# Performance work log

Measured on AMD Instinct MI355X. Metric: run time of the kernel, lower is better.

Reference implementation:

```python
import jax, jax.numpy as jnp
import numpy as np

SCALE = 20.0
EPS = 1e-8  # matches torch F.cosine_similarity eps


def _l2_normalize(x):
    # torch cosine_similarity clamps norms at eps
    norm = jnp.maximum(jnp.linalg.norm(x, axis=-1, keepdims=True), EPS)
    return x / norm


def setup_inputs() -> dict:
    key = jax.random.key(0)
    k1, k2 = jax.random.split(key)
    B, D = 4096, 1024
    anchor_emb = jax.random.normal(k1, (B, D), dtype=jnp.float32)
    pos_negs_emb = jax.random.normal(k2, (B, D), dtype=jnp.float32)
    return {"anchor_emb": anchor_emb, "pos_negs_emb": pos_negs_emb}


def reference(anchor_emb, pos_negs_emb):
    # cosine similarity as normalized GEMM (avoids (B,N,D) broadcast intermediate)
    a = _l2_normalize(anchor_emb)            # [B, D]
    p = _l2_normalize(pos_negs_emb)          # [N, D]
    scores = SCALE * jnp.einsum("bd,nd->bn", a, p)  # [B, N]
    B = scores.shape[0]
    # cross entropy with labels = arange(B): mean(logsumexp - diag)
    logZ = jax.scipy.special.logsumexp(scores, axis=1)  # [B]
    diag = scores[jnp.arange(B), jnp.arange(B)]          # [B]
    return jnp.mean(logZ - diag)
```

## Files before the change

### kernel.cpp

```cpp
#include <hip/hip_runtime.h>
#include <math.h>

#define NB 4096
#define ND 1024
#define SCALEF 20.0f
#define SQ 448.0f

typedef int intx4 __attribute__((ext_vector_type(4)));

__device__ __forceinline__ void load16_to_lds(const void* g, void* l) {
    __builtin_amdgcn_global_load_lds(
        (const __attribute__((address_space(1))) void*)g,
        (__attribute__((address_space(3))) void*)l, 16, 0, 0);
}

__device__ __forceinline__ int q8(float x) {
    float c = fminf(fmaxf(x, -127.0f), 127.0f);
    return (int)rintf(c);
}

__global__ __launch_bounds__(256) void mnrl_norm_cvt(
    const float* __restrict__ A, const float* __restrict__ P,
    signed char* __restrict__ Aq, signed char* __restrict__ Pq,
    float* __restrict__ rowsum, float* __restrict__ out) {
    if (blockIdx.x == 0 && threadIdx.x == 0) out[0] = 0.0f;
    int row = blockIdx.x * 4 + (threadIdx.x >> 6);
    int lane = threadIdx.x & 63;
    bool is_a = row < NB;
    const float* src = is_a ? (A + (size_t)row * ND)
                            : (P + (size_t)(row - NB) * ND);
    unsigned int* dst = (unsigned int*)(is_a ? (Aq + (size_t)row * ND)
                                             : (Pq + (size_t)(row - NB) * ND));

    float4 v[4];
    float ss = 0.0f;
#pragma unroll
    for (int i = 0; i < 4; ++i) {
        v[i] = ((const float4*)src)[i * 64 + lane];
        ss += v[i].x * v[i].x + v[i].y * v[i].y + v[i].z * v[i].z + v[i].w * v[i].w;
    }
#pragma unroll
    for (int off = 32; off > 0; off >>= 1) ss += __shfl_xor(ss, off, 64);
    float inv = SQ / fmaxf(sqrtf(ss), 1e-8f);
#pragma unroll
    for (int i = 0; i < 4; ++i) {
        int q0 = q8(v[i].x * inv), q1 = q8(v[i].y * inv);
        int q2 = q8(v[i].z * inv), q3 = q8(v[i].w * inv);
        dst[i * 64 + lane] = (unsigned int)((q0 & 255) | ((q1 & 255) << 8) |
                                            ((q2 & 255) << 16) | (q3 << 24));
    }
    if (is_a && lane == 0) rowsum[row] = 0.0f;
}

__global__ __launch_bounds__(512, 2) void mnrl_gemm_lse(
    const signed char* __restrict__ Aq, const signed char* __restrict__ Pq,
    float* __restrict__ rowsum, float* __restrict__ diag) {
    __shared__ __align__(16) unsigned char lds_a[2][256 * 128];
    __shared__ __align__(16) unsigned char lds_b[2][256 * 128];

    int bid = blockIdx.x;
    int swz = (bid & 7) * 32 + (bid >> 3);
    int tile_m = swz >> 4;
    int tile_n = swz & 15;

    int t = threadIdx.x;
    int lane = t & 63;
    int w = t >> 6;
    int wm = w >> 2;
    int wn = w & 3;
    int quad = lane >> 4;
    int l16 = lane & 15;

    const signed char* Abase = Aq + (size_t)tile_m * 256 * ND;
    const signed char* Pbase = Pq + (size_t)tile_n * 256 * ND;

    int srow = lane >> 3;
    int schunk = (lane & 7) ^ srow;
    const signed char* sA = Abase + (size_t)(w * 32 + srow) * ND + schunk * 16;
    const signed char* sP = Pbase + (size_t)(w * 32 + srow) * ND + schunk * 16;
    const int sdst = w * 4096;

    int e7 = l16 & 7;
    int aRow = (wm * 128 + l16) * 128;
    int bRow = (wn * 64 + l16) * 128;

    intx4 acc[8][4];
#pragma unroll
    for (int mt = 0; mt < 8; ++mt)
#pragma unroll
        for (int nt = 0; nt < 4; ++nt) acc[mt][nt] = (intx4){0, 0, 0, 0};

#define STAGE(KT)                                                            \
    {                                                                        \
        int ko_ = (KT) * 128;                                                \
        int b_ = (KT) & 1;                                                   \
        _Pragma("unroll") for (int j = 0; j < 4; ++j) {                      \
            load16_to_lds(sA + (size_t)j * 8 * ND + ko_,                     \
                          &lds_a[b_][sdst + j * 1024]);                      \
            load16_to_lds(sP + (size_t)j * 8 * ND + ko_,                     \
                          &lds_b[b_][sdst + j * 1024]);                      \
        }                                                                    \
    }

    STAGE(0);

    for (int kt = 0; kt < 8; ++kt) {
        asm volatile("s_waitcnt vmcnt(0)" ::: "memory");
        __builtin_amdgcn_s_barrier();
        asm volatile("" ::: "memory");
        if (kt < 7) STAGE(kt + 1);
        const unsigned char* ba = &lds_a[kt & 1][0];
        const unsigned char* bb = &lds_b[kt & 1][0];
#pragma unroll
        for (int s = 0; s < 2; ++s) {
            int so = ((s * 4 + quad) ^ e7) * 16;
            intx4 af[8], bv[4];
#pragma unroll
            for (int mt = 0; mt < 8; ++mt)
                af[mt] = *(const intx4*)&ba[aRow + mt * 2048 + so];
#pragma unroll
            for (int nt = 0; nt < 4; ++nt)
                bv[nt] = *(const intx4*)&bb[bRow + nt * 2048 + so];
            __builtin_amdgcn_s_setprio(1);
#pragma unroll
            for (int mt = 0; mt < 8; ++mt)
#pragma unroll
                for (int nt = 0; nt < 4; ++nt)
                    acc[mt][nt] = __builtin_amdgcn_mfma_i32_16x16x64_i8(
                        af[mt], bv[nt], acc[mt][nt], 0, 0, 0);
            __builtin_amdgcn_s_setprio(0);
        }
    }
#undef STAGE

    const float SC = SCALEF / (SQ * SQ);
    bool diag_block = (tile_m == tile_n);
    float psum[8][4];
#pragma unroll
    for (int mt = 0; mt < 8; ++mt)
#pragma unroll
        for (int r = 0; r < 4; ++r) psum[mt][r] = 0.0f;

#pragma unroll
    for (int mt = 0; mt < 8; ++mt)
#pragma unroll
        for (int nt = 0; nt < 4; ++nt)
#pragma unroll
            for (int r = 0; r < 4; ++r) {
                float sc = SC * (float)acc[mt][nt][r];
                psum[mt][r] += __expf(sc - SCALEF);
                if (diag_block) {
                    int rt = wm * 128 + mt * 16 + quad * 4 + r;
                    int ct = wn * 64 + nt * 16 + l16;
                    if (rt == ct) diag[tile_m * 256 + rt] = sc;
                }
            }

    float* part = (float*)&lds_a[0][0];
#pragma unroll
    for (int mt = 0; mt < 8; ++mt)
#pragma unroll
        for (int r = 0; r < 4; ++r) {
            float v = psum[mt][r];
            v += __shfl_xor(v, 1, 64);
            v += __shfl_xor(v, 2, 64);
            v += __shfl_xor(v, 4, 64);
            v += __shfl_xor(v, 8, 64);
            if (l16 == 0) part[wn * 256 + wm * 128 + mt * 16 + quad * 4 + r] = v;
        }
    __syncthreads();
    if (t < 256) {
        float s = part[t] + part[256 + t] + part[512 + t] + part[768 + t];
        atomicAdd(&rowsum[tile_m * 256 + t], s);
    }
}

__global__ __launch_bounds__(256) void mnrl_finalize(const float* __restrict__ rowsum,
                                                     const float* __restrict__ diag,
                                                     float* __restrict__ out) {
    int t = threadIdx.x;
    int i = blockIdx.x * 256 + t;
    float local = (logf(rowsum[i]) + SCALEF) - diag[i];
#pragma unroll
    for (int off = 32; off > 0; off >>= 1) local += __shfl_down(local, off, 64);
    __shared__ float sred[4];
    if ((t & 63) == 0) sred[t >> 6] = local;
    __syncthreads();
    if (t == 0)
        atomicAdd(out, (sred[0] + sred[1] + sred[2] + sred[3]) * (1.0f / (float)NB));
}

extern "C" void kernel_launch(void* const* d_in, const int* in_sizes, int n_in,
                              void* d_out, int out_size, void* d_ws, size_t ws_size,
                              hipStream_t stream) {
    const float* A = (const float*)d_in[0];
    const float* P = (const float*)d_in[1];

    signed char* Aq = (signed char*)d_ws;
    signed char* Pq = Aq + (size_t)NB * ND;
    float* rowsum = (float*)(Pq + (size_t)NB * ND);
    float* diag = rowsum + NB;

    mnrl_norm_cvt<<<2 * NB / 4, 256, 0, stream>>>(A, P, Aq, Pq, rowsum,
                                                  (float*)d_out);
    mnrl_gemm_lse<<<16 * 16, 512, 0, stream>>>(Aq, Pq, rowsum, diag);
    mnrl_finalize<<<16, 256, 0, stream>>>(rowsum, diag, (float*)d_out);
}
```

Before: 100.9 us.

## Shrink GEMM tile to 256x128 with K-step 64 to double block count

The int8 GEMM+LSE kernel moves from 256x256 tiles with a 128-deep K step to 256x128 tiles with a 64-deep K step. That doubles the grid to 512 blocks, quarters the LDS footprint, and raises the occupancy hint to 4 blocks per CU. The LDS swizzle, warp layout, diagonal extraction and partial row-sum reduction are all reworked to match. The aim is to fill more CUs on the 256-CU part and hide latency better. The cost is lower data reuse per block, more barriers per K iteration, and twice as many atomic row-sum updates.

Result: no change. 99.03 us, median of 2 (-1.8%).

```diff
diff --git a/kernel.cpp b/kernel.cpp
--- a/kernel.cpp
+++ b/kernel.cpp
@@ -52,97 +52,97 @@
     if (is_a && lane == 0) rowsum[row] = 0.0f;
 }
 
-__global__ __launch_bounds__(512, 2) void mnrl_gemm_lse(
+__global__ __launch_bounds__(512, 4) void mnrl_gemm_lse(
     const signed char* __restrict__ Aq, const signed char* __restrict__ Pq,
     float* __restrict__ rowsum, float* __restrict__ diag) {
-    __shared__ __align__(16) unsigned char lds_a[2][256 * 128];
-    __shared__ __align__(16) unsigned char lds_b[2][256 * 128];
+    __shared__ __align__(16) unsigned char lds_a[2][256 * 64];
+    __shared__ __align__(16) unsigned char lds_b[2][128 * 64];
 
     int bid = blockIdx.x;
-    int swz = (bid & 7) * 32 + (bid >> 3);
-    int tile_m = swz >> 4;
-    int tile_n = swz & 15;
+    int swz = (bid & 7) * 64 + (bid >> 3);
+    int tile_m = swz >> 5;
+    int tile_n = swz & 31;
 
     int t = threadIdx.x;
     int lane = t & 63;
     int w = t >> 6;
-    int wm = w >> 2;
-    int wn = w & 3;
+    int wm = w >> 1;
+    int wn = w & 1;
     int quad = lane >> 4;
     int l16 = lane & 15;
 
     const signed char* Abase = Aq + (size_t)tile_m * 256 * ND;
-    const signed char* Pbase = Pq + (size_t)tile_n * 256 * ND;
-
-    int srow = lane >> 3;
-    int schunk = (lane & 7) ^ srow;
-    const signed char* sA = Abase + (size_t)(w * 32 + srow) * ND + schunk * 16;
-    const signed char* sP = Pbase + (size_t)(w * 32 + srow) * ND + schunk * 16;
-    const int sdst = w * 4096;
-
-    int e7 = l16 & 7;
-    int aRow = (wm * 128 + l16) * 128;
-    int bRow = (wn * 64 + l16) * 128;
-
-    intx4 acc[8][4];
-#pragma unroll
-    for (int mt = 0; mt < 8; ++mt)
+    const signed char* Pbase = Pq + (size_t)tile_n * 128 * ND;
+
+    int srow = lane >> 2;
+    int chunk = (lane & 3) ^ ((lane >> 3) & 3);
+    const signed char* srcA0 = Abase + (size_t)(w * 32 + srow) * ND + chunk * 16;
+    const signed char* srcA1 = srcA0 + (size_t)16 * ND;
+    const signed char* srcP0 = Pbase + (size_t)(w * 16 + srow) * ND + chunk * 16;
+    const int dstA0 = w * 2048;
+    const int dstA1 = w * 2048 + 1024;
+    const int dstP = w * 1024;
+
+    int slot16 = (quad ^ ((l16 >> 1) & 3)) * 16;
+    int offA[4], offB[4];
+#pragma unroll
+    for (int mt = 0; mt < 4; ++mt)
+        offA[mt] = (wm * 64 + mt * 16 + l16) * 64 + slot16;
+#pragma unroll
+    for (int nt = 0; nt < 4; ++nt)
+        offB[nt] = (wn * 64 + nt * 16 + l16) * 64 + slot16;
+
+    intx4 acc[4][4];
+#pragma unroll
+    for (int mt = 0; mt < 4; ++mt)
 #pragma unroll
         for (int nt = 0; nt < 4; ++nt) acc[mt][nt] = (intx4){0, 0, 0, 0};
 
-#define STAGE(KT)                                                            \
-    {                                                                        \
-        int ko_ = (KT) * 128;                                                \
-        int b_ = (KT) & 1;                                                   \
-        _Pragma("unroll") for (int j = 0; j < 4; ++j) {                      \
-            load16_to_lds(sA + (size_t)j * 8 * ND + ko_,                     \
-                          &lds_a[b_][sdst + j * 1024]);                      \
-            load16_to_lds(sP + (size_t)j * 8 * ND + ko_,                     \
-                          &lds_b[b_][sdst + j * 1024]);                      \
-        }                                                                    \
+#define STAGE(KT)                                                   \
+    {                                                               \
+        int koff_ = (KT) * 64;                                      \
+        int b_ = (KT) & 1;                                          \
+        load16_to_lds(srcA0 + koff_, &lds_a[b_][dstA0]);            \
+        load16_to_lds(srcA1 + koff_, &lds_a[b_][dstA1]);            \
+        load16_to_lds(srcP0 + koff_, &lds_b[b_][dstP]);             \
     }
 
     STAGE(0);
 
-    for (int kt = 0; kt < 8; ++kt) {
+    for (int kt = 0; kt < 16; ++kt) {
         asm volatile("s_waitcnt vmcnt(0)" ::: "memory");
         __builtin_amdgcn_s_barrier();
         asm volatile("" ::: "memory");
-        if (kt < 7) STAGE(kt + 1);
+        if (kt < 15) STAGE(kt + 1);
         const unsigned char* ba = &lds_a[kt & 1][0];
         const unsigned char* bb = &lds_b[kt & 1][0];
-#pragma unroll
-        for (int s = 0; s < 2; ++s) {
-            int so = ((s * 4 + quad) ^ e7) * 16;
-            intx4 af[8], bv[4];
-#pragma unroll
-            for (int mt = 0; mt < 8; ++mt)
-                af[mt] = *(const intx4*)&ba[aRow + mt * 2048 + so];
+        intx4 af[4], bv[4];
+#pragma unroll
+        for (int mt = 0; mt < 4; ++mt) af[mt] = *(const intx4*)&ba[offA[mt]];
+#pragma unroll
+        for (int nt = 0; nt < 4; ++nt) bv[nt] = *(const intx4*)&bb[offB[nt]];
+        __builtin_amdgcn_s_setprio(1);
+#pragma unroll
+        for (int mt = 0; mt < 4; ++mt)
 #pragma unroll
             for (int nt = 0; nt < 4; ++nt)
-                bv[nt] = *(const intx4*)&bb[bRow + nt * 2048 + so];
-            __builtin_amdgcn_s_setprio(1);
-#pragma unroll
-            for (int mt = 0; mt < 8; ++mt)
-#pragma unroll
-                for (int nt = 0; nt < 4; ++nt)
-                    acc[mt][nt] = __builtin_amdgcn_mfma_i32_16x16x64_i8(
-                        af[mt], bv[nt], acc[mt][nt], 0, 0, 0);
-            __builtin_amdgcn_s_setprio(0);
-        }
+                acc[mt][nt] = __builtin_amdgcn_mfma_i32_16x16x64_i8(
+                    af[mt], bv[nt], acc[mt][nt], 0, 0, 0);
+        __builtin_amdgcn_s_setprio(0);
     }
 #undef STAGE
 
     const float SC = SCALEF / (SQ * SQ);
-    bool diag_block = (tile_m == tile_n);
-    float psum[8][4];
-#pragma unroll
-    for (int mt = 0; mt < 8; ++mt)
+    bool diag_block = ((tile_n >> 1) == tile_m);
+    int coff = (tile_n & 1) * 128;
+    float psum[4][4];
+#pragma unroll
+    for (int mt = 0; mt < 4; ++mt)
 #pragma unroll
         for (int r = 0; r < 4; ++r) psum[mt][r] = 0.0f;
 
 #pragma unroll
-    for (int mt = 0; mt < 8; ++mt)
+    for (int mt = 0; mt < 4; ++mt)
 #pragma unroll
         for (int nt = 0; nt < 4; ++nt)
 #pragma unroll
@@ -150,15 +150,15 @@
                 float sc = SC * (float)acc[mt][nt][r];
                 psum[mt][r] += __expf(sc - SCALEF);
                 if (diag_block) {
-                    int rt = wm * 128 + mt * 16 + quad * 4 + r;
+                    int rt = wm * 64 + mt * 16 + quad * 4 + r;
                     int ct = wn * 64 + nt * 16 + l16;
-                    if (rt == ct) diag[tile_m * 256 + rt] = sc;
+                    if (rt == ct + coff) diag[tile_m * 256 + rt] = sc;
                 }
             }
 
     float* part = (float*)&lds_a[0][0];
 #pragma unroll
-    for (int mt = 0; mt < 8; ++mt)
+    for (int mt = 0; mt < 4; ++mt)
 #pragma unroll
         for (int r = 0; r < 4; ++r) {
             float v = psum[mt][r];
@@ -166,11 +166,11 @@
             v += __shfl_xor(v, 2, 64);
             v += __shfl_xor(v, 4, 64);
             v += __shfl_xor(v, 8, 64);
-            if (l16 == 0) part[wn * 256 + wm * 128 + mt * 16 + quad * 4 + r] = v;
+            if (l16 == 0) part[wn * 256 + wm * 64 + mt * 16 + quad * 4 + r] = v;
         }
     __syncthreads();
     if (t < 256) {
-        float s = part[t] + part[256 + t] + part[512 + t] + part[768 + t];
+        float s = part[t] + part[256 + t];
         atomicAdd(&rowsum[tile_m * 256 + t], s);
     }
 }
@@ -203,6 +203,6 @@
 
     mnrl_norm_cvt<<<2 * NB / 4, 256, 0, stream>>>(A, P, Aq, Pq, rowsum,
                                                   (float*)d_out);
-    mnrl_gemm_lse<<<16 * 16, 512, 0, stream>>>(Aq, Pq, rowsum, diag);
+    mnrl_gemm_lse<<<16 * 32, 512, 0, stream>>>(Aq, Pq, rowsum, diag);
     mnrl_finalize<<<16, 256, 0, stream>>>(rowsum, diag, (float*)d_out);
 }
```
